# Optimization experiments

Measured on AMD Instinct MI355X. Metric: run time of the kernel, lower is better.

## Reference

```python
import jax, jax.numpy as jnp
import numpy as np

B, T, I, H, L, O = 32, 2048, 256, 512, 2, 64


def _gru_layer(x, Wi, bi, Wh, bhn):
    """Flax GRUCell semantics. x: (B,T,in). Wi:(in,3H) bi:(3H) Wh:(H,3H) bhn:(H).
    Gate order along the 3H axis: [r, z, n]."""
    Hd = Wh.shape[0]
    # Precompute all input-side projections at once (one big GEMM).
    xi = jnp.einsum('bti,ih->bth', x, Wi) + bi  # (B,T,3H)

    def step(h, xt):
        hh = h @ Wh  # (B,3H), hidden-side denses (no bias except hn)
        r = jax.nn.sigmoid(xt[:, :Hd] + hh[:, :Hd])
        z = jax.nn.sigmoid(xt[:, Hd:2 * Hd] + hh[:, Hd:2 * Hd])
        n = jnp.tanh(xt[:, 2 * Hd:] + r * (hh[:, 2 * Hd:] + bhn))
        h_new = (1.0 - z) * n + z * h
        return h_new, h_new

    h0 = jnp.zeros((x.shape[0], Hd), dtype=x.dtype)
    _, ys = jax.lax.scan(step, h0, jnp.swapaxes(xi, 0, 1))  # ys: (T,B,H)
    return jnp.swapaxes(ys, 0, 1)  # (B,T,H)


def setup_inputs() -> dict:
    key = jax.random.key(0)
    ks = jax.random.split(key, 11)
    si, sh = 1.0 / np.sqrt(I), 1.0 / np.sqrt(H)
    return {
        'x': jax.random.normal(ks[0], (B, T, I), dtype=jnp.float32),
        'Wi0': jax.random.normal(ks[1], (I, 3 * H), jnp.float32) * si,
        'bi0': jnp.zeros((3 * H,), jnp.float32),
        'Wh0': jax.random.normal(ks[2], (H, 3 * H), jnp.float32) * sh,
        'bhn0': jnp.zeros((H,), jnp.float32),
        'Wi1': jax.random.normal(ks[3], (H, 3 * H), jnp.float32) * sh,
        'bi1': jnp.zeros((3 * H,), jnp.float32),
        'Wh1': jax.random.normal(ks[4], (H, 3 * H), jnp.float32) * sh,
        'bhn1': jnp.zeros((H,), jnp.float32),
        'Wfc': jax.random.normal(ks[5], (H, O), jnp.float32) * sh,
        'bfc': jnp.zeros((O,), jnp.float32),
        'deterministic': 1,
    }


def reference(x, Wi0, bi0, Wh0, bhn0, Wi1, bi1, Wh1, bhn1, Wfc, bfc, deterministic):
    # deterministic=1 -> dropout is identity (matches deterministic=True).
    h = _gru_layer(x, Wi0, bi0, Wh0, bhn0)   # layer 0
    h = _gru_layer(h, Wi1, bi1, Wh1, bhn1)   # layer 1 (dropout skipped: deterministic)
    return h[:, -1, :] @ Wfc + bfc           # (B, O)
```

## Files before the change

kernel.cpp:

```cpp
#include <hip/hip_runtime.h>


typedef unsigned int  u32;
typedef unsigned short u16;
typedef float v4f __attribute__((ext_vector_type(4)));
typedef _Float16 v2h __attribute__((ext_vector_type(2)));
typedef _Float16 v8h __attribute__((ext_vector_type(8)));

#if defined(__has_builtin)
#  if __has_builtin(__builtin_amdgcn_fdot2)
#    define FDOT2(a, b, c) __builtin_amdgcn_fdot2((a), (b), (c), false)
#  endif
#endif
#ifndef FDOT2
#  define FDOT2(a, b, c) ((c) + (float)(a)[0] * (float)(b)[0] + (float)(a)[1] * (float)(b)[1])
#endif

__device__ __forceinline__ u16 f2h(float f) {
    _Float16 h = (_Float16)f;
    return *(u16*)&h;
}
__device__ __forceinline__ float h2f(u16 b) {
    _Float16 h = *(_Float16*)&b;
    return (float)h;
}


__global__ __launch_bounds__(256) void transpose_cast(const float* __restrict__ src,
                                                      u16* __restrict__ dst,
                                                      int R, int C) {
    __shared__ u16 tile[32][33];
    int c0 = blockIdx.x * 32, r0 = blockIdx.y * 32;
    int t = threadIdx.x;
    {
        int rl = t >> 3, cl4 = (t & 7) * 4;
        float4 v = *(const float4*)&src[(size_t)(r0 + rl) * C + c0 + cl4];
        tile[rl][cl4 + 0] = f2h(v.x);
        tile[rl][cl4 + 1] = f2h(v.y);
        tile[rl][cl4 + 2] = f2h(v.z);
        tile[rl][cl4 + 3] = f2h(v.w);
    }
    __syncthreads();
    {
        int cl = t >> 3, rl4 = (t & 7) * 4;
        uint2 o;
        o.x = (u32)tile[rl4 + 0][cl] | ((u32)tile[rl4 + 1][cl] << 16);
        o.y = (u32)tile[rl4 + 2][cl] | ((u32)tile[rl4 + 3][cl] << 16);
        *(uint2*)&dst[(size_t)(c0 + cl) * R + r0 + rl4] = o;
    }
}

__global__ __launch_bounds__(256) void pack_wh(const float* __restrict__ Wh,
                                               uint4* __restrict__ dst) {
    int id = blockIdx.x * 256 + threadIdx.x;
    int l = id & 63;
    int c = (id >> 6) % 24;
    int mw = id / 1536;
    int m = mw >> 3, w = mw & 7;
    int g = c >> 3, qk = c & 7;
    int col = g * 512 + m * 64 + l;
    int kb = w * 64 + qk * 8;
    u32 d[4];
#pragma unroll
    for (int p = 0; p < 4; ++p) {
        u16 a = f2h(Wh[(size_t)(kb + 2 * p) * 1536 + col]);
        u16 b = f2h(Wh[(size_t)(kb + 2 * p + 1) * 1536 + col]);
        d[p] = (u32)a | ((u32)b << 16);
    }
    uint4 o; o.x = d[0]; o.y = d[1]; o.z = d[2]; o.w = d[3];
    dst[id] = o;
}

template <int K, bool AF32>
__global__ __launch_bounds__(256) void gemm_xi(const void* __restrict__ Ap,
                                               const u16* __restrict__ Bt,
                                               const float* __restrict__ bias,
                                               u16* __restrict__ C,
                                               int t0, int lgTc) {
    __shared__ u16 As[64 * 40];
    __shared__ u16 Bs[64 * 40];
    const int tid = threadIdx.x;
    const int n0 = blockIdx.x * 64;
    const int m0 = blockIdx.y * 64;
    const int row = tid >> 2, koff = (tid & 3) * 8;
    const int lane = tid & 63, w = tid >> 6;
    const int m = m0 + row;
    const int b = m >> lgTc;
    const int tl = m & ((1 << lgTc) - 1);
    const size_t srow = ((size_t)b << 11) + (size_t)(t0 + tl);
    v4f acc[4];
#pragma unroll
    for (int i = 0; i < 4; ++i) acc[i] = (v4f){0.f, 0.f, 0.f, 0.f};

    for (int k0 = 0; k0 < K; k0 += 32) {
        if (AF32) {
            const float* A = (const float*)Ap;
            float4 v0 = *(const float4*)&A[srow * K + k0 + koff];
            float4 v1 = *(const float4*)&A[srow * K + k0 + koff + 4];
            uint4 o;
            o.x = (u32)f2h(v0.x) | ((u32)f2h(v0.y) << 16);
            o.y = (u32)f2h(v0.z) | ((u32)f2h(v0.w) << 16);
            o.z = (u32)f2h(v1.x) | ((u32)f2h(v1.y) << 16);
            o.w = (u32)f2h(v1.z) | ((u32)f2h(v1.w) << 16);
            *(uint4*)&As[row * 40 + koff] = o;
        } else {
            const u16* A = (const u16*)Ap;
            *(uint4*)&As[row * 40 + koff] =
                *(const uint4*)&A[srow * K + k0 + koff];
        }
        *(uint4*)&Bs[row * 40 + koff] =
            *(const uint4*)&Bt[(size_t)(n0 + row) * K + k0 + koff];
        __syncthreads();
        v8h a = *(const v8h*)&As[(w * 16 + (lane & 15)) * 40 + (lane >> 4) * 8];
#pragma unroll
        for (int nt = 0; nt < 4; ++nt) {
            v8h bm = *(const v8h*)&Bs[(nt * 16 + (lane & 15)) * 40 + (lane >> 4) * 8];
            acc[nt] = __builtin_amdgcn_mfma_f32_16x16x32_f16(a, bm, acc[nt], 0, 0, 0);
        }
        __syncthreads();
    }
#pragma unroll
    for (int nt = 0; nt < 4; ++nt) {
        int col = n0 + nt * 16 + (lane & 15);
        float bv = bias[col];
#pragma unroll
        for (int rI = 0; rI < 4; ++rI) {
            int rowm = m0 + w * 16 + (lane >> 4) * 4 + rI;
            C[(size_t)rowm * 1536 + col] = f2h(acc[nt][rI] + bv);
        }
    }
}

__global__ __launch_bounds__(576) void gru_scan(const u16* __restrict__ xi,
                                                const uint4* __restrict__ Whp,
                                                const float* __restrict__ bhn,
                                                u32* __restrict__ Hb,
                                                u16* __restrict__ hseq,
                                                float* __restrict__ h1last,
                                                float* __restrict__ hstate,
                                                int t0, int Tc, int layer0) {
    __shared__ __align__(16) u16 Sh[8][64];
    __shared__ float P[2][8][3][64];
    __shared__ u32 flagP[2][8];

    const int tid = threadIdx.x;
    const int wg = blockIdx.x;
    const int cluster = wg & 31;
    const int member = wg >> 5;
    const int W = tid >> 6, lane = tid & 63;
    const int bg = cluster;

    if (tid < 16) ((u32*)flagP)[tid] = 0;

    if (W < 8) {
        uint4 Wreg[24];
        {
            const uint4* src = Whp + ((size_t)(member * 8 + W) * 24) * 64 + lane;
#pragma unroll
            for (int c = 0; c < 24; ++c) Wreg[c] = src[c * 64];
        }
        __syncthreads();

        u32* pollbase = Hb + (size_t)cluster * 1024 + W * 64 + lane;
        for (int t = t0; t < t0 + Tc; ++t) {
            u16 hv = 0;
            if (t > 0) {
                u32* myq = pollbase + ((t - 1) & 1) * 512;
                const u32 target = (u32)(u16)t << 16;
                u32 qv = 0;
                for (int it = 0; it < 4000000; ++it) {
                    qv = __hip_atomic_load(myq, __ATOMIC_RELAXED, __HIP_MEMORY_SCOPE_AGENT);
                    if ((qv & 0xFFFF0000u) == target) break;
                    if (it > 2) __builtin_amdgcn_s_sleep(1);
                }
                hv = (u16)qv;
            }
            Sh[W][lane] = hv;

            float a0 = 0.f, a1 = 0.f, a2 = 0.f;
#pragma unroll
            for (int qk = 0; qk < 8; ++qk) {
                v8h h8 = *(const v8h*)&Sh[W][qk * 8];
                const v2h* hp = (const v2h*)&h8;
                v8h w0 = *(const v8h*)&Wreg[qk];
                v8h w1 = *(const v8h*)&Wreg[8 + qk];
                v8h w2 = *(const v8h*)&Wreg[16 + qk];
                const v2h* p0 = (const v2h*)&w0;
                const v2h* p1 = (const v2h*)&w1;
                const v2h* p2 = (const v2h*)&w2;
#pragma unroll
                for (int p = 0; p < 4; ++p) {
                    a0 = FDOT2(p0[p], hp[p], a0);
                    a1 = FDOT2(p1[p], hp[p], a1);
                    a2 = FDOT2(p2[p], hp[p], a2);
                }
            }
            const int pp = t & 1;
            P[pp][W][0][lane] = a0;
            P[pp][W][1][lane] = a1;
            P[pp][W][2][lane] = a2;
            if (lane == 0)
                __hip_atomic_store(&flagP[pp][W], (u32)(t + 1), __ATOMIC_RELEASE,
                                   __HIP_MEMORY_SCOPE_WORKGROUP);
        }
    } else {
        const int j = member * 64 + lane;
        float bhnv = bhn[j];
        float hprev = (t0 > 0) ? hstate[bg * 512 + j] : 0.f;
        const u16* xp = xi + (size_t)bg * Tc * 1536 + j;
        u16 rx = xp[0], rz = xp[512], rn = xp[1024];
        __syncthreads();

        u32* slotj = Hb + (size_t)cluster * 1024 + j;
        for (int t = t0; t < t0 + Tc; ++t) {
            const int pp = t & 1;
            for (int it = 0; it < 4000000; ++it) {
                u32 v = __hip_atomic_load(&flagP[pp][lane & 7], __ATOMIC_ACQUIRE,
                                          __HIP_MEMORY_SCOPE_WORKGROUP);
                if (__all(v == (u32)(t + 1))) break;
                if (it > 8) __builtin_amdgcn_s_sleep(1);
            }
            float a0 = 0.f, a1 = 0.f, a2 = 0.f;
#pragma unroll
            for (int w = 0; w < 8; ++w) {
                a0 += P[pp][w][0][lane];
                a1 += P[pp][w][1][lane];
                a2 += P[pp][w][2][lane];
            }
            float r = 1.f / (1.f + __expf(-(h2f(rx) + a0)));
            float z = 1.f / (1.f + __expf(-(h2f(rz) + a1)));
            float nx = h2f(rn) + r * (a2 + bhnv);
            float n = 1.f - 2.f / (__expf(2.f * nx) + 1.f);
            float hn = (1.f - z) * n + z * hprev;
            hprev = hn;
            u16 hh = f2h(hn);
            __hip_atomic_store(&slotj[pp * 512], ((u32)(u16)(t + 1) << 16) | (u32)hh,
                               __ATOMIC_RELAXED, __HIP_MEMORY_SCOPE_AGENT);
            if (layer0) hseq[((size_t)bg * 2048 + t) * 512 + j] = hh;
            if (!layer0 && t == 2047) h1last[bg * 512 + j] = hn;
            if (t + 1 < t0 + Tc) {
                const u16* p = xi + ((size_t)bg * Tc + (t + 1 - t0)) * 1536 + j;
                rx = p[0]; rz = p[512]; rn = p[1024];
            }
        }
        hstate[bg * 512 + j] = hprev;
    }
}

__global__ __launch_bounds__(64) void final_fc(const float* __restrict__ h1,
                                               const float* __restrict__ Wfc,
                                               const float* __restrict__ bfc,
                                               float* __restrict__ out) {
    int b = blockIdx.x, o = threadIdx.x;
    float acc = bfc[o];
    for (int k = 0; k < 512; ++k) acc += h1[b * 512 + k] * Wfc[k * 64 + o];
    out[b * 64 + o] = acc;
}


extern "C" void kernel_launch(void* const* d_in, const int* in_sizes, int n_in,
                              void* d_out, int out_size, void* d_ws, size_t ws_size,
                              hipStream_t stream) {
    const float* x    = (const float*)d_in[0];
    const float* Wi0  = (const float*)d_in[1];
    const float* bi0  = (const float*)d_in[2];
    const float* Wh0  = (const float*)d_in[3];
    const float* bhn0 = (const float*)d_in[4];
    const float* Wi1  = (const float*)d_in[5];
    const float* bi1  = (const float*)d_in[6];
    const float* Wh1  = (const float*)d_in[7];
    const float* bhn1 = (const float*)d_in[8];
    const float* Wfc  = (const float*)d_in[9];
    const float* bfc  = (const float*)d_in[10];
    float* out = (float*)d_out;
    (void)in_sizes; (void)n_in; (void)out_size;

    char* ws = (char*)d_ws;
    size_t off = 0;
    auto take = [&](size_t bytes) -> char* {
        char* p = ws + off;
        off = (off + bytes + 255) & ~(size_t)255;
        return p;
    };
    u16*  Wi0t  = (u16*)take(1536 * 256 * 2);
    u16*  Wi1t  = (u16*)take(1536 * 512 * 2);
    uint4* Wh0p = (uint4*)take(98304 * 16);
    uint4* Wh1p = (uint4*)take(98304 * 16);
    u32*  Hb0   = (u32*)take(32 * 1024 * 4);
    u32*  Hb1   = (u32*)take(32 * 1024 * 4);
    float* hstate = (float*)take(32 * 512 * 4);
    float* h1last = (float*)take(32 * 512 * 4);
    u16*  h0seq = (u16*)take((size_t)32 * 2048 * 512 * 2);
    size_t fixed_end = off;

    int Tc = 2048;
    if (ws_size > 0) {
        while (Tc > 128 &&
               fixed_end + (size_t)32 * Tc * 1536 * 2 > ws_size) Tc >>= 1;
    }
    int lgTc = 31 - __builtin_clz((u32)Tc);
    u16* xibuf = (u16*)take((size_t)32 * Tc * 1536 * 2);
    int nChunk = 2048 / Tc;

    transpose_cast<<<dim3(48, 8), 256, 0, stream>>>(Wi0, Wi0t, 256, 1536);
    transpose_cast<<<dim3(48, 16), 256, 0, stream>>>(Wi1, Wi1t, 512, 1536);
    pack_wh<<<384, 256, 0, stream>>>(Wh0, Wh0p);
    pack_wh<<<384, 256, 0, stream>>>(Wh1, Wh1p);

    for (int c = 0; c < nChunk; ++c) {
        int t0 = c * Tc;
        gemm_xi<256, true><<<dim3(24, Tc / 2), 256, 0, stream>>>(
            (const void*)x, Wi0t, bi0, xibuf, t0, lgTc);
        const u16* xi_p = xibuf; const uint4* wh_p = Wh0p; const float* bh_p = bhn0;
        u32* hb_p = Hb0; u16* hs_p = h0seq; float* h1_p = nullptr;
        float* st_p = hstate; int t0v = t0, Tcv = Tc, l0v = 1;
        void* args[] = {&xi_p, &wh_p, &bh_p, &hb_p, &hs_p, &h1_p, &st_p,
                        &t0v, &Tcv, &l0v};
        hipLaunchCooperativeKernel(gru_scan, dim3(256), dim3(576), args, 0, stream);
    }
    for (int c = 0; c < nChunk; ++c) {
        int t0 = c * Tc;
        gemm_xi<512, false><<<dim3(24, Tc / 2), 256, 0, stream>>>(
            (const void*)h0seq, Wi1t, bi1, xibuf, t0, lgTc);
        const u16* xi_p = xibuf; const uint4* wh_p = Wh1p; const float* bh_p = bhn1;
        u32* hb_p = Hb1; u16* hs_p = nullptr; float* h1_p = h1last;
        float* st_p = hstate; int t0v = t0, Tcv = Tc, l0v = 0;
        void* args[] = {&xi_p, &wh_p, &bh_p, &hb_p, &hs_p, &h1_p, &st_p,
                        &t0v, &Tcv, &l0v};
        hipLaunchCooperativeKernel(gru_scan, dim3(256), dim3(576), args, 0, stream);
    }
    final_fc<<<32, 64, 0, stream>>>(h1last, Wfc, bfc, out);
}
```

Measured before the change: 6.654 ms.

## Fuse both GRU layers into one wavefront-pipelined persistent scan kernel

Replaces the two sequential per-layer scans with one cooperative kernel. 64 workgroups run layer 0 and 128 run layer 1, which lags one step behind and computes its input projection on the fly from layer 0's hidden state. This drops the layer-1 input GEMM, the full h0 sequence write and read, and one serial scan over time. In exchange it adds a 4-deep hidden-state ring, cross-layer progress flags for backpressure, and heavier per-step polling. Each workgroup now handles 4 batch rows with K split across lane halves.

```diff
diff --git a/kernel.cpp b/kernel.cpp
--- a/kernel.cpp
+++ b/kernel.cpp
@@ -23,6 +23,9 @@
 __device__ __forceinline__ float h2f(u16 b) {
     _Float16 h = *(_Float16*)&b;
     return (float)h;
+}
+__device__ __forceinline__ u32 LDG(const u32* p) {
+    return __hip_atomic_load(p, __ATOMIC_RELAXED, __HIP_MEMORY_SCOPE_AGENT);
 }
 
 
@@ -60,6 +63,27 @@
     int g = c >> 3, qk = c & 7;
     int col = g * 512 + m * 64 + l;
     int kb = w * 64 + qk * 8;
+    u32 d[4];
+#pragma unroll
+    for (int p = 0; p < 4; ++p) {
+        u16 a = f2h(Wh[(size_t)(kb + 2 * p) * 1536 + col]);
+        u16 b = f2h(Wh[(size_t)(kb + 2 * p + 1) * 1536 + col]);
+        d[p] = (u32)a | ((u32)b << 16);
+    }
+    uint4 o; o.x = d[0]; o.y = d[1]; o.z = d[2]; o.w = d[3];
+    dst[id] = o;
+}
+
+__global__ __launch_bounds__(256) void pack_whB(const float* __restrict__ Wh,
+                                                uint4* __restrict__ dst) {
+    int id = blockIdx.x * 256 + threadIdx.x;
+    int l = id & 63;
+    int c = (id >> 6) % 12;
+    int mw = id / 768;
+    int mB = mw >> 3, w = mw & 7;
+    int g = c >> 2, qk4 = c & 3;
+    int col = g * 512 + mB * 32 + (l & 31);
+    int kb = w * 64 + (l >> 5) * 32 + qk4 * 8;
     u32 d[4];
 #pragma unroll
     for (int p = 0; p < 4; ++p) {
@@ -131,119 +155,293 @@
     }
 }
 
-__global__ __launch_bounds__(576) void gru_scan(const u16* __restrict__ xi,
-                                                const uint4* __restrict__ Whp,
-                                                const float* __restrict__ bhn,
-                                                u32* __restrict__ Hb,
-                                                u16* __restrict__ hseq,
-                                                float* __restrict__ h1last,
-                                                float* __restrict__ hstate,
-                                                int t0, int Tc, int layer0) {
-    __shared__ __align__(16) u16 Sh[8][64];
-    __shared__ float P[2][8][3][64];
-    __shared__ u32 flagP[2][8];
+__global__ __launch_bounds__(512) void gru_scan2(const u16* __restrict__ xi,
+                                                 const uint4* __restrict__ Wh0p,
+                                                 const uint4* __restrict__ Wh1B,
+                                                 const uint4* __restrict__ Wi1B,
+                                                 const float* __restrict__ bi1,
+                                                 const float* __restrict__ bhn0,
+                                                 const float* __restrict__ bhn1,
+                                                 u32* __restrict__ Hb0,
+                                                 u32* __restrict__ Hb1,
+                                                 u32* __restrict__ ProgA,
+                                                 u32* __restrict__ Prog1,
+                                                 float* __restrict__ h1last,
+                                                 float* __restrict__ hstate0,
+                                                 float* __restrict__ hstate1,
+                                                 int t0, int Tc) {
+    struct SA {
+        u16 Sh[4][8][64];
+        float P0[2][4][8][3][64];
+        u32 flag[2][4][8];
+    };
+    struct SB {
+        u16 Sh1[4][8][64];
+        u16 Sh0[4][8][64];
+        float P1[2][4][8][6][32];
+        u32 flag[2][4][8];
+    };
+    union SU { SA a; SB b; };
+    __shared__ __align__(16) SU S;
 
     const int tid = threadIdx.x;
     const int wg = blockIdx.x;
-    const int cluster = wg & 31;
-    const int member = wg >> 5;
+    const int mc = wg / 24;
+    const int rr = wg % 24;
     const int W = tid >> 6, lane = tid & 63;
-    const int bg = cluster;
-
-    if (tid < 16) ((u32*)flagP)[tid] = 0;
-
-    if (W < 8) {
+    const int tEnd = t0 + Tc;
+
+    if (rr < 8) {
+        const int m = rr;
+        if (tid < 64) ((u32*)S.a.flag)[tid] = 0;
         uint4 Wreg[24];
         {
-            const uint4* src = Whp + ((size_t)(member * 8 + W) * 24) * 64 + lane;
+            const uint4* src = Wh0p + ((size_t)(m * 8 + W) * 24) * 64 + lane;
 #pragma unroll
             for (int c = 0; c < 24; ++c) Wreg[c] = src[c * 64];
         }
+        const int j = m * 64 + lane;
+        const int bq = mc * 4 + W;
+        float bhnv = 0.f, hprev = 0.f;
+        u16 rx = 0, rz = 0, rn = 0;
+        const u32* gp = ProgA;
+        u32 pgv = 0;
+        if (W < 4) {
+            bhnv = bhn0[j];
+            if (t0 > 0) hprev = hstate0[bq * 512 + j];
+            const u16* p = xi + ((size_t)bq * Tc) * 1536 + j;
+            rx = p[0]; rz = p[512]; rn = p[1024];
+            gp = (lane < 8)  ? (ProgA + bq * 8 + lane)
+               : (lane < 24) ? (Prog1 + bq * 16 + (lane - 8))
+                             : (ProgA + bq * 8);
+            pgv = LDG(gp);
+        }
         __syncthreads();
 
-        u32* pollbase = Hb + (size_t)cluster * 1024 + W * 64 + lane;
-        for (int t = t0; t < t0 + Tc; ++t) {
-            u16 hv = 0;
-            if (t > 0) {
-                u32* myq = pollbase + ((t - 1) & 1) * 512;
-                const u32 target = (u32)(u16)t << 16;
-                u32 qv = 0;
-                for (int it = 0; it < 4000000; ++it) {
-                    qv = __hip_atomic_load(myq, __ATOMIC_RELAXED, __HIP_MEMORY_SCOPE_AGENT);
-                    if ((qv & 0xFFFF0000u) == target) break;
-                    if (it > 2) __builtin_amdgcn_s_sleep(1);
-                }
-                hv = (u16)qv;
+        for (int t = t0; t < tEnd; ++t) {
+            const int pp = t & 1;
+#pragma unroll
+            for (int q = 0; q < 4; ++q) {
+                u16 hv = 0;
+                if (t > 0) {
+                    const u32 tg = (u32)(u16)t << 16;
+                    const u32* p = Hb0 + (size_t)(mc * 4 + q) * 2048 +
+                                   ((t - 1) & 3) * 512 + W * 64 + lane;
+                    u32 v = 0;
+                    for (int it = 0; it < 2000000; ++it) {
+                        v = LDG(p);
+                        if ((v & 0xFFFF0000u) == tg) break;
+                        if (it > 16) __builtin_amdgcn_s_sleep(1);
+                    }
+                    hv = (u16)v;
+                }
+                S.a.Sh[q][W][lane] = hv;
+                float a0 = 0.f, a1 = 0.f, a2 = 0.f;
+#pragma unroll
+                for (int qk = 0; qk < 8; ++qk) {
+                    v8h h8 = *(const v8h*)&S.a.Sh[q][W][qk * 8];
+                    const v2h* hp = (const v2h*)&h8;
+                    const v2h* p0 = (const v2h*)&Wreg[qk];
+                    const v2h* p1 = (const v2h*)&Wreg[8 + qk];
+                    const v2h* p2 = (const v2h*)&Wreg[16 + qk];
+#pragma unroll
+                    for (int p = 0; p < 4; ++p) {
+                        a0 = FDOT2(p0[p], hp[p], a0);
+                        a1 = FDOT2(p1[p], hp[p], a1);
+                        a2 = FDOT2(p2[p], hp[p], a2);
+                    }
+                }
+                S.a.P0[pp][q][W][0][lane] = a0;
+                S.a.P0[pp][q][W][1][lane] = a1;
+                S.a.P0[pp][q][W][2][lane] = a2;
+                if (lane == 0)
+                    __hip_atomic_store(&S.a.flag[pp][q][W], (u32)(t + 1),
+                                       __ATOMIC_RELEASE, __HIP_MEMORY_SCOPE_WORKGROUP);
+                if (W == q) {
+                    for (int it = 0; it < 2000000; ++it) {
+                        u32 fv = __hip_atomic_load(&S.a.flag[pp][q][lane & 7],
+                                                   __ATOMIC_ACQUIRE, __HIP_MEMORY_SCOPE_WORKGROUP);
+                        if (__all((lane >= 8) | (fv == (u32)(t + 1)))) break;
+                        if (it > 16) __builtin_amdgcn_s_sleep(1);
+                    }
+                    float s0 = 0.f, s1 = 0.f, s2 = 0.f;
+#pragma unroll
+                    for (int w2 = 0; w2 < 8; ++w2) {
+                        s0 += S.a.P0[pp][q][w2][0][lane];
+                        s1 += S.a.P0[pp][q][w2][1][lane];
+                        s2 += S.a.P0[pp][q][w2][2][lane];
+                    }
+                    float r = 1.f / (1.f + __expf(-(h2f(rx) + s0)));
+                    float z = 1.f / (1.f + __expf(-(h2f(rz) + s1)));
+                    float nx = h2f(rn) + r * (s2 + bhnv);
+                    float n = 1.f - 2.f / (__expf(2.f * nx) + 1.f);
+                    float hn = (1.f - z) * n + z * hprev;
+                    hprev = hn;
+                    if (t >= 4) {
+                        const int thr = (lane < 8) ? (t - 3) : (t - 4);
+                        if (!__all((lane >= 24) || ((int)pgv >= thr))) {
+                            for (int it = 0; it < 2000000; ++it) {
+                                pgv = LDG(gp);
+                                if (__all((lane >= 24) || ((int)pgv >= thr))) break;
+                                if (it > 8) __builtin_amdgcn_s_sleep(1);
+                            }
+                        }
+                    }
+                    __hip_atomic_store(Hb0 + (size_t)bq * 2048 + (t & 3) * 512 + j,
+                                       ((u32)(u16)(t + 1) << 16) | (u32)f2h(hn),
+                                       __ATOMIC_RELAXED, __HIP_MEMORY_SCOPE_AGENT);
+                    if (lane == 0)
+                        __hip_atomic_store(ProgA + bq * 8 + m, (u32)t,
+                                           __ATOMIC_RELAXED, __HIP_MEMORY_SCOPE_AGENT);
+                    pgv = LDG(gp);
+                    if (t + 1 < tEnd) {
+                        const u16* p = xi + ((size_t)bq * Tc + (t + 1 - t0)) * 1536 + j;
+                        rx = p[0]; rz = p[512]; rn = p[1024];
+                    }
+                }
             }
-            Sh[W][lane] = hv;
-
-            float a0 = 0.f, a1 = 0.f, a2 = 0.f;
-#pragma unroll
-            for (int qk = 0; qk < 8; ++qk) {
-                v8h h8 = *(const v8h*)&Sh[W][qk * 8];
-                const v2h* hp = (const v2h*)&h8;
-                v8h w0 = *(const v8h*)&Wreg[qk];
-                v8h w1 = *(const v8h*)&Wreg[8 + qk];
-                v8h w2 = *(const v8h*)&Wreg[16 + qk];
-                const v2h* p0 = (const v2h*)&w0;
-                const v2h* p1 = (const v2h*)&w1;
-                const v2h* p2 = (const v2h*)&w2;
-#pragma unroll
-                for (int p = 0; p < 4; ++p) {
-                    a0 = FDOT2(p0[p], hp[p], a0);
-                    a1 = FDOT2(p1[p], hp[p], a1);
-                    a2 = FDOT2(p2[p], hp[p], a2);
+        }
+        if (W < 4) hstate0[bq * 512 + j] = hprev;
+    } else {
+        const int mB = rr - 8;
+        if (tid < 64) ((u32*)S.b.flag)[tid] = 0;
+        uint4 Hreg[12], Xreg[12];
+        {
+            const uint4* hs = Wh1B + ((size_t)(mB * 8 + W) * 12) * 64 + lane;
+            const uint4* xs = Wi1B + ((size_t)(mB * 8 + W) * 12) * 64 + lane;
+#pragma unroll
+            for (int c = 0; c < 12; ++c) { Hreg[c] = hs[c * 64]; Xreg[c] = xs[c * 64]; }
+        }
+        const int jB = mB * 32 + (lane & 31);
+        const int kloc = (lane >> 5) * 32;
+        const float b_r = bi1[jB], b_z = bi1[512 + jB], b_n = bi1[1024 + jB];
+        const float bh = bhn1[jB];
+        const int bq = mc * 4 + W;
+        float hprev = 0.f;
+        if (W < 4 && t0 > 0) hprev = hstate1[bq * 512 + jB];
+        __syncthreads();
+
+        for (int t = t0; t < tEnd; ++t) {
+            const int pp = t & 1;
+#pragma unroll
+            for (int q = 0; q < 4; ++q) {
+                u16 hv = 0;
+                if (t > 0) {
+                    const u32 tg = (u32)(u16)t << 16;
+                    const u32* p = Hb1 + (size_t)(mc * 4 + q) * 1024 +
+                                   ((t - 1) & 1) * 512 + W * 64 + lane;
+                    u32 v = 0;
+                    for (int it = 0; it < 2000000; ++it) {
+                        v = LDG(p);
+                        if ((v & 0xFFFF0000u) == tg) break;
+                        if (it > 16) __builtin_amdgcn_s_sleep(1);
+                    }
+                    hv = (u16)v;
+                }
+                S.b.Sh1[q][W][lane] = hv;
+                float a0 = 0.f, a1 = 0.f, a2 = 0.f;
+#pragma unroll
+                for (int qk = 0; qk < 4; ++qk) {
+                    v8h h8 = *(const v8h*)&S.b.Sh1[q][W][kloc + qk * 8];
+                    const v2h* hp = (const v2h*)&h8;
+                    const v2h* p0 = (const v2h*)&Hreg[qk];
+                    const v2h* p1 = (const v2h*)&Hreg[4 + qk];
+                    const v2h* p2 = (const v2h*)&Hreg[8 + qk];
+#pragma unroll
+                    for (int p = 0; p < 4; ++p) {
+                        a0 = FDOT2(p0[p], hp[p], a0);
+                        a1 = FDOT2(p1[p], hp[p], a1);
+                        a2 = FDOT2(p2[p], hp[p], a2);
+                    }
+                }
+                a0 += __shfl_xor(a0, 32);
+                a1 += __shfl_xor(a1, 32);
+                a2 += __shfl_xor(a2, 32);
+                if (lane < 32) {
+                    S.b.P1[pp][q][W][0][lane] = a0;
+                    S.b.P1[pp][q][W][1][lane] = a1;
+                    S.b.P1[pp][q][W][2][lane] = a2;
                 }
             }
-            const int pp = t & 1;
-            P[pp][W][0][lane] = a0;
-            P[pp][W][1][lane] = a1;
-            P[pp][W][2][lane] = a2;
-            if (lane == 0)
-                __hip_atomic_store(&flagP[pp][W], (u32)(t + 1), __ATOMIC_RELEASE,
-                                   __HIP_MEMORY_SCOPE_WORKGROUP);
-        }
-    } else {
-        const int j = member * 64 + lane;
-        float bhnv = bhn[j];
-        float hprev = (t0 > 0) ? hstate[bg * 512 + j] : 0.f;
-        const u16* xp = xi + (size_t)bg * Tc * 1536 + j;
-        u16 rx = xp[0], rz = xp[512], rn = xp[1024];
-        __syncthreads();
-
-        u32* slotj = Hb + (size_t)cluster * 1024 + j;
-        for (int t = t0; t < t0 + Tc; ++t) {
-            const int pp = t & 1;
-            for (int it = 0; it < 4000000; ++it) {
-                u32 v = __hip_atomic_load(&flagP[pp][lane & 7], __ATOMIC_ACQUIRE,
-                                          __HIP_MEMORY_SCOPE_WORKGROUP);
-                if (__all(v == (u32)(t + 1))) break;
-                if (it > 8) __builtin_amdgcn_s_sleep(1);
+#pragma unroll
+            for (int q = 0; q < 4; ++q) {
+                u16 hv = 0;
+                {
+                    const u32 tg = (u32)(u16)(t + 1) << 16;
+                    const u32* p = Hb0 + (size_t)(mc * 4 + q) * 2048 +
+                                   (t & 3) * 512 + W * 64 + lane;
+                    u32 v = 0;
+                    for (int it = 0; it < 2000000; ++it) {
+                        v = LDG(p);
+                        if ((v & 0xFFFF0000u) == tg) break;
+                        if (it > 16) __builtin_amdgcn_s_sleep(1);
+                    }
+                    hv = (u16)v;
+                }
+                S.b.Sh0[q][W][lane] = hv;
+                float a0 = 0.f, a1 = 0.f, a2 = 0.f;
+#pragma unroll
+                for (int qk = 0; qk < 4; ++qk) {
+                    v8h h8 = *(const v8h*)&S.b.Sh0[q][W][kloc + qk * 8];
+                    const v2h* hp = (const v2h*)&h8;
+                    const v2h* p0 = (const v2h*)&Xreg[qk];
+                    const v2h* p1 = (const v2h*)&Xreg[4 + qk];
+                    const v2h* p2 = (const v2h*)&Xreg[8 + qk];
+#pragma unroll
+                    for (int p = 0; p < 4; ++p) {
+                        a0 = FDOT2(p0[p], hp[p], a0);
+                        a1 = FDOT2(p1[p], hp[p], a1);
+                        a2 = FDOT2(p2[p], hp[p], a2);
+                    }
+                }
+                a0 += __shfl_xor(a0, 32);
+                a1 += __shfl_xor(a1, 32);
+                a2 += __shfl_xor(a2, 32);
+                if (lane < 32) {
+                    S.b.P1[pp][q][W][3][lane] = a0;
+                    S.b.P1[pp][q][W][4][lane] = a1;
+                    S.b.P1[pp][q][W][5][lane] = a2;
+                }
+                if (lane == 0)
+                    __hip_atomic_store(&S.b.flag[pp][q][W], (u32)(t + 1),
+                                       __ATOMIC_RELEASE, __HIP_MEMORY_SCOPE_WORKGROUP);
+                if (W == q) {
+                    for (int it = 0; it < 2000000; ++it) {
+                        u32 fv = __hip_atomic_load(&S.b.flag[pp][q][lane & 7],
+                                                   __ATOMIC_ACQUIRE, __HIP_MEMORY_SCOPE_WORKGROUP);
+                        if (__all((lane >= 8) | (fv == (u32)(t + 1)))) break;
+                        if (it > 16) __builtin_amdgcn_s_sleep(1);
+                    }
+                    const int lj = lane & 31;
+                    float HR = 0.f, HZ = 0.f, HN = 0.f, XR = 0.f, XZ = 0.f, XN = 0.f;
+#pragma unroll
+                    for (int w2 = 0; w2 < 8; ++w2) {
+                        HR += S.b.P1[pp][q][w2][0][lj];
+                        HZ += S.b.P1[pp][q][w2][1][lj];
+                        HN += S.b.P1[pp][q][w2][2][lj];
+                        XR += S.b.P1[pp][q][w2][3][lj];
+                        XZ += S.b.P1[pp][q][w2][4][lj];
+                        XN += S.b.P1[pp][q][w2][5][lj];
+                    }
+                    if (lane < 32) {
+                        float r = 1.f / (1.f + __expf(-(XR + b_r + HR)));
+                        float z = 1.f / (1.f + __expf(-(XZ + b_z + HZ)));
+                        float nx = XN + b_n + r * (HN + bh);
+                        float n = 1.f - 2.f / (__expf(2.f * nx) + 1.f);
+                        float hn = (1.f - z) * n + z * hprev;
+                        hprev = hn;
+                        __hip_atomic_store(Hb1 + (size_t)bq * 1024 + (t & 1) * 512 + jB,
+                                           ((u32)(u16)(t + 1) << 16) | (u32)f2h(hn),
+                                           __ATOMIC_RELAXED, __HIP_MEMORY_SCOPE_AGENT);
+                        if (t == 2047) h1last[bq * 512 + jB] = hn;
+                    }
+                    if (lane == 0)
+                        __hip_atomic_store(Prog1 + bq * 16 + mB, (u32)t,
+                                           __ATOMIC_RELAXED, __HIP_MEMORY_SCOPE_AGENT);
+                }
             }
-            float a0 = 0.f, a1 = 0.f, a2 = 0.f;
-#pragma unroll
-            for (int w = 0; w < 8; ++w) {
-                a0 += P[pp][w][0][lane];
-                a1 += P[pp][w][1][lane];
-                a2 += P[pp][w][2][lane];
-            }
-            float r = 1.f / (1.f + __expf(-(h2f(rx) + a0)));
-            float z = 1.f / (1.f + __expf(-(h2f(rz) + a1)));
-            float nx = h2f(rn) + r * (a2 + bhnv);
-            float n = 1.f - 2.f / (__expf(2.f * nx) + 1.f);
-            float hn = (1.f - z) * n + z * hprev;
-            hprev = hn;
-            u16 hh = f2h(hn);
-            __hip_atomic_store(&slotj[pp * 512], ((u32)(u16)(t + 1) << 16) | (u32)hh,
-                               __ATOMIC_RELAXED, __HIP_MEMORY_SCOPE_AGENT);
-            if (layer0) hseq[((size_t)bg * 2048 + t) * 512 + j] = hh;
-            if (!layer0 && t == 2047) h1last[bg * 512 + j] = hn;
-            if (t + 1 < t0 + Tc) {
-                const u16* p = xi + ((size_t)bg * Tc + (t + 1 - t0)) * 1536 + j;
-                rx = p[0]; rz = p[512]; rn = p[1024];
-            }
-        }
-        hstate[bg * 512 + j] = hprev;
+        }
+        if (W < 4 && lane < 32) hstate1[bq * 512 + jB] = hprev;
     }
 }
 
@@ -283,14 +481,16 @@
         return p;
     };
     u16*  Wi0t  = (u16*)take(1536 * 256 * 2);
-    u16*  Wi1t  = (u16*)take(1536 * 512 * 2);
     uint4* Wh0p = (uint4*)take(98304 * 16);
-    uint4* Wh1p = (uint4*)take(98304 * 16);
-    u32*  Hb0   = (u32*)take(32 * 1024 * 4);
+    uint4* Wh1B = (uint4*)take(98304 * 16);
+    uint4* Wi1B = (uint4*)take(98304 * 16);
+    u32*  Hb0   = (u32*)take(32 * 2048 * 4);
     u32*  Hb1   = (u32*)take(32 * 1024 * 4);
-    float* hstate = (float*)take(32 * 512 * 4);
-    float* h1last = (float*)take(32 * 512 * 4);
-    u16*  h0seq = (u16*)take((size_t)32 * 2048 * 512 * 2);
+    u32*  ProgA = (u32*)take(32 * 8 * 4);
+    u32*  Prog1 = (u32*)take(32 * 16 * 4);
+    float* hstate0 = (float*)take(32 * 512 * 4);
+    float* hstate1 = (float*)take(32 * 512 * 4);
+    float* h1last  = (float*)take(32 * 512 * 4);
     size_t fixed_end = off;
 
     int Tc = 2048;
@@ -302,32 +502,30 @@
     u16* xibuf = (u16*)take((size_t)32 * Tc * 1536 * 2);
     int nChunk = 2048 / Tc;
 
+    hipMemsetAsync(Hb0, 0, 32 * 2048 * 4, stream);
+    hipMemsetAsync(Hb1, 0, 32 * 1024 * 4, stream);
+    hipMemsetAsync(ProgA, 0, 32 * 8 * 4, stream);
+    hipMemsetAsync(Prog1, 0, 32 * 16 * 4, stream);
+
     transpose_cast<<<dim3(48, 8), 256, 0, stream>>>(Wi0, Wi0t, 256, 1536);
-    transpose_cast<<<dim3(48, 16), 256, 0, stream>>>(Wi1, Wi1t, 512, 1536);
     pack_wh<<<384, 256, 0, stream>>>(Wh0, Wh0p);
-    pack_wh<<<384, 256, 0, stream>>>(Wh1, Wh1p);
+    pack_whB<<<384, 256, 0, stream>>>(Wh1, Wh1B);
+    pack_whB<<<384, 256, 0, stream>>>(Wi1, Wi1B);
 
     for (int c = 0; c < nChunk; ++c) {
         int t0 = c * Tc;
         gemm_xi<256, true><<<dim3(24, Tc / 2), 256, 0, stream>>>(
             (const void*)x, Wi0t, bi0, xibuf, t0, lgTc);
-        const u16* xi_p = xibuf; const uint4* wh_p = Wh0p; const float* bh_p = bhn0;
-        u32* hb_p = Hb0; u16* hs_p = h0seq; float* h1_p = nullptr;
-        float* st_p = hstate; int t0v = t0, Tcv = Tc, l0v = 1;
-        void* args[] = {&xi_p, &wh_p, &bh_p, &hb_p, &hs_p, &h1_p, &st_p,
-                        &t0v, &Tcv, &l0v};
-        hipLaunchCooperativeKernel(gru_scan, dim3(256), dim3(576), args, 0, stream);
-    }
-    for (int c = 0; c < nChunk; ++c) {
-        int t0 = c * Tc;
-        gemm_xi<512, false><<<dim3(24, Tc / 2), 256, 0, stream>>>(
-            (const void*)h0seq, Wi1t, bi1, xibuf, t0, lgTc);
-        const u16* xi_p = xibuf; const uint4* wh_p = Wh1p; const float* bh_p = bhn1;
-        u32* hb_p = Hb1; u16* hs_p = nullptr; float* h1_p = h1last;
-        float* st_p = hstate; int t0v = t0, Tcv = Tc, l0v = 0;
-        void* args[] = {&xi_p, &wh_p, &bh_p, &hb_p, &hs_p, &h1_p, &st_p,
-                        &t0v, &Tcv, &l0v};
-        hipLaunchCooperativeKernel(gru_scan, dim3(256), dim3(576), args, 0, stream);
+        const u16* xi_p = xibuf;
+        const uint4* wh0_p = Wh0p; const uint4* wh1_p = Wh1B; const uint4* wi1_p = Wi1B;
+        const float* bi1_p = bi1; const float* bh0_p = bhn0; const float* bh1_p = bhn1;
+        u32* hb0_p = Hb0; u32* hb1_p = Hb1; u32* pga_p = ProgA; u32* pg1_p = Prog1;
+        float* h1l_p = h1last; float* st0_p = hstate0; float* st1_p = hstate1;
+        int t0v = t0, Tcv = Tc;
+        void* args[] = {&xi_p, &wh0_p, &wh1_p, &wi1_p, &bi1_p, &bh0_p, &bh1_p,
+                        &hb0_p, &hb1_p, &pga_p, &pg1_p, &h1l_p, &st0_p, &st1_p,
+                        &t0v, &Tcv};
+        hipLaunchCooperativeKernel(gru_scan2, dim3(192), dim3(512), args, 0, stream);
     }
     final_fc<<<32, 64, 0, stream>>>(h1last, Wfc, bfc, out);
 }
```

After: 13.88 ms. 2.09x slower.
